# Performance work log

Hardware: AMD Instinct MI355X
Metric: run time of the kernel (lower is better)

Reference implementation:

```python
import jax, jax.numpy as jnp
import numpy as np

B = 16384
H = 1024

def setup_inputs() -> dict:
    key = jax.random.key(0)
    k1, k2, k3, k4, k5 = jax.random.split(key, 5)
    inp = jax.random.normal(k1, (B, 3 * H), dtype=jnp.float32)
    previous_state = jax.random.normal(k2, (B, H), dtype=jnp.float32)
    mask = jax.random.uniform(k3, (B,), dtype=jnp.float32)
    # params: th_normal scale 0.08
    Wur = 0.08 * jax.random.normal(k4, (H, 2 * H), dtype=jnp.float32)
    U = 0.08 * jax.random.normal(k5, (H, H), dtype=jnp.float32)
    return {"inp": inp, "previous_state": previous_state, "mask": mask, "Wur": Wur, "U": U}

def reference(inp, previous_state, mask, Wur, U):
    h = U.shape[0]
    state_inp = inp[:, :h]            # [B, H]
    gate_inp = inp[:, h:]             # [B, 2H]
    gates = jax.nn.sigmoid(previous_state @ Wur + gate_inp)  # [B, 2H]
    update = gates[:, :h]
    reset = gates[:, h:]
    p = (state_inp * reset) @ U       # [B, H]
    next_state = jnp.tanh(p + state_inp)
    # NOTE: faithful to source (additive combine, not convex blend)
    next_state_f = next_state + update + (previous_state + (1.0 - update))
    m = mask[:, None]
    return m * next_state_f + (1.0 - m) * previous_state
```

## Files before the change

### kernel.cpp

```cpp
#include <hip/hip_runtime.h>
#include <cstdint>
#include <cstddef>

#define DI __device__ __forceinline__

typedef __attribute__((ext_vector_type(8))) short short8;
typedef __attribute__((ext_vector_type(4))) float floatx4;

static constexpr int BATCH = 16384;
static constexpr int H = 1024;

DI unsigned short f32_to_bf16_bits(float x) {
  union { float f; unsigned int u; } c; c.f = x;
  unsigned int r = c.u + 0x7fffu + ((c.u >> 16) & 1u);
  return (unsigned short)(r >> 16);
}

__global__ __launch_bounds__(256) void cast_bf16_kernel(const float* __restrict__ in,
                                                        unsigned short* __restrict__ out) {
  const int i = (blockIdx.x * 256 + threadIdx.x) * 8;
  const float4 v0 = *reinterpret_cast<const float4*>(in + i);
  const float4 v1 = *reinterpret_cast<const float4*>(in + i + 4);
  short8 o;
  o[0] = (short)f32_to_bf16_bits(v0.x);
  o[1] = (short)f32_to_bf16_bits(v0.y);
  o[2] = (short)f32_to_bf16_bits(v0.z);
  o[3] = (short)f32_to_bf16_bits(v0.w);
  o[4] = (short)f32_to_bf16_bits(v1.x);
  o[5] = (short)f32_to_bf16_bits(v1.y);
  o[6] = (short)f32_to_bf16_bits(v1.z);
  o[7] = (short)f32_to_bf16_bits(v1.w);
  *reinterpret_cast<short8*>(out + i) = o;
}

__global__ __launch_bounds__(256) void transpose_cast2_kernel(const float* __restrict__ Wur,
                                                              const float* __restrict__ U,
                                                              unsigned short* __restrict__ WrT,
                                                              unsigned short* __restrict__ UT) {
  __shared__ float tile[32][33];
  const float* in;
  unsigned short* out;
  int src_stride, src_col0;
  if (blockIdx.z == 0) {
    in = Wur; out = WrT; src_stride = 2 * H; src_col0 = H;
  } else {
    in = U; out = UT; src_stride = H; src_col0 = 0;
  }
  const int bx = blockIdx.x * 32;
  const int by = blockIdx.y * 32;
  const int tx = threadIdx.x;
  const int ty = threadIdx.y;
#pragma unroll
  for (int i = 0; i < 32; i += 8)
    tile[ty + i][tx] = in[(size_t)(bx + ty + i) * src_stride + src_col0 + by + tx];
  __syncthreads();
#pragma unroll
  for (int i = 0; i < 32; i += 8)
    out[(size_t)(by + ty + i) * H + bx + tx] = f32_to_bf16_bits(tile[tx][ty + i]);
}

template <int EPI>
__global__ __launch_bounds__(256, 3) void gemm_fused(const unsigned short* __restrict__ A,
                                                     const unsigned short* __restrict__ Bt,
                                                     const float* __restrict__ inp,
                                                     const float* __restrict__ prev,
                                                     const float* __restrict__ mask,
                                                     unsigned short* __restrict__ Xout,
                                                     float* __restrict__ Out) {
  __shared__ __align__(16) unsigned short ldsA[128 * 64];
  __shared__ __align__(16) unsigned short ldsB[128 * 64];

  const int tid = threadIdx.x;
  const int lane = tid & 63;
  const int wave = tid >> 6;
  const int wm = wave >> 1;
  const int wn = wave & 1;
  const int q = lane >> 4;
  const int l16 = lane & 15;

  const int sid = blockIdx.y * gridDim.x + blockIdx.x;
  const int nwg = gridDim.x * gridDim.y;
  const int lid = (sid & 7) * (nwg >> 3) + (sid >> 3);
  const int bx = lid & 7;
  const int by = lid >> 3;
  const int blockM = by * 128;
  const int blockN = bx * 128;

  floatx4 acc[4][4] = {};

  for (int kt = 0; kt < H; kt += 64) {
#pragma unroll
    for (int j = 0; j < 4; ++j) {
      const int c = j * 256 + tid;
      const int r = c >> 3;
      const int gc = (c & 7) ^ (r & 7);
      const int cb = j * 256 + (wave << 6);
      const unsigned short* srcA = A + (size_t)(blockM + r) * H + kt + gc * 8;
      const unsigned short* srcB = Bt + (size_t)(blockN + r) * H + kt + gc * 8;
#if __has_builtin(__builtin_amdgcn_global_load_lds)
      __builtin_amdgcn_global_load_lds(
          (const __attribute__((address_space(1))) unsigned int*)srcA,
          (__attribute__((address_space(3))) unsigned int*)(&ldsA[cb * 8]), 16, 0, 0);
      __builtin_amdgcn_global_load_lds(
          (const __attribute__((address_space(1))) unsigned int*)srcB,
          (__attribute__((address_space(3))) unsigned int*)(&ldsB[cb * 8]), 16, 0, 0);
#else
      *(short8*)&ldsA[c * 8] = *(const short8*)srcA;
      *(short8*)&ldsB[c * 8] = *(const short8*)srcB;
#endif
    }
#if __has_builtin(__builtin_amdgcn_global_load_lds)
    asm volatile("s_waitcnt vmcnt(0)" ::: "memory");
#endif
    __syncthreads();

#pragma unroll
    for (int ks = 0; ks < 2; ++ks) {
      short8 af[4], bfr[4];
#pragma unroll
      for (int i = 0; i < 4; ++i) {
        const int r = wm * 64 + i * 16 + l16;
        const int ch = ks * 4 + q;
        af[i] = *(const short8*)&ldsA[(r * 8 + (ch ^ (r & 7))) * 8];
      }
#pragma unroll
      for (int j = 0; j < 4; ++j) {
        const int r = wn * 64 + j * 16 + l16;
        const int ch = ks * 4 + q;
        bfr[j] = *(const short8*)&ldsB[(r * 8 + (ch ^ (r & 7))) * 8];
      }
#pragma unroll
      for (int i = 0; i < 4; ++i)
#pragma unroll
        for (int j = 0; j < 4; ++j)
          acc[i][j] = __builtin_amdgcn_mfma_f32_16x16x32_bf16(af[i], bfr[j], acc[i][j], 0, 0, 0);
    }
    __syncthreads();
  }

#pragma unroll
  for (int i = 0; i < 4; ++i) {
    const int gr0 = blockM + wm * 64 + i * 16 + q * 4;
#pragma unroll
    for (int j = 0; j < 4; ++j) {
      const int gcol = blockN + wn * 64 + j * 16 + l16;
#pragma unroll
      for (int rg = 0; rg < 4; ++rg) {
        const int gr = gr0 + rg;
        const float v = acc[i][j][rg];
        if (EPI == 0) {
          const float z = v + inp[(size_t)gr * (3 * H) + 2 * H + gcol];
          const float rst = 1.0f / (1.0f + __expf(-z));
          const float x = inp[(size_t)gr * (3 * H) + gcol] * rst;
          Xout[(size_t)gr * H + gcol] = f32_to_bf16_bits(x);
        } else {
          const float s = inp[(size_t)gr * (3 * H) + gcol];
          const float a = v + s;
          const float ns = 1.0f - 2.0f / (__expf(2.0f * a) + 1.0f);
          const float m = mask[gr];
          Out[(size_t)gr * H + gcol] = m * (ns + 1.0f) + prev[(size_t)gr * H + gcol];
        }
      }
    }
  }
}

extern "C" void kernel_launch(void* const* d_in, const int* in_sizes, int n_in,
                              void* d_out, int out_size, void* d_ws, size_t ws_size,
                              hipStream_t stream) {
  const float* inp = (const float*)d_in[0];
  const float* prev = (const float*)d_in[1];
  const float* mask = (const float*)d_in[2];
  const float* Wur = (const float*)d_in[3];
  const float* U = (const float*)d_in[4];
  float* out = (float*)d_out;

  char* ws = (char*)d_ws;
  unsigned short* prevb = (unsigned short*)ws;
  unsigned short* Xb = (unsigned short*)(ws + (size_t)BATCH * H * 2);
  unsigned short* WrT = (unsigned short*)(ws + (size_t)BATCH * H * 4);
  unsigned short* UT = WrT + (size_t)H * H;

  cast_bf16_kernel<<<(BATCH * H) / (256 * 8), 256, 0, stream>>>(prev, prevb);
  transpose_cast2_kernel<<<dim3(H / 32, H / 32, 2), dim3(32, 8), 0, stream>>>(Wur, U, WrT, UT);

  gemm_fused<0><<<dim3(H / 128, BATCH / 128), 256, 0, stream>>>(prevb, WrT, inp, nullptr,
                                                                nullptr, Xb, nullptr);
  gemm_fused<1><<<dim3(H / 128, BATCH / 128), 256, 0, stream>>>(Xb, UT, inp, prev, mask,
                                                                nullptr, out);
}
```

Before: 427.2 us.

## Use 256x256 tiles with double-buffered LDS and interleaved load/MFMA phases

The GEMM kernels move from 128x128 tiles with 4 waves to 256x256 tiles with 8 waves. The LDS is now double-buffered and filled by direct global-to-LDS loads, so each K step overlaps the prefetch of the next tile with four MFMA quadrant phases. Those phases are separated by barriers and raised wave priority (setprio). The aim is more data reuse per tile and hidden load latency, at the cost of more registers (32 accumulators), 128KB of LDS, fewer workgroups and more barriers. Occupancy and tail effects may change as a result.

```diff
diff --git a/kernel.cpp b/kernel.cpp
--- a/kernel.cpp
+++ b/kernel.cpp
@@ -9,6 +9,8 @@
 
 static constexpr int BATCH = 16384;
 static constexpr int H = 1024;
+static constexpr int NT = H / 64;
+static constexpr int HALF = 128 * 64;
 
 DI unsigned short f32_to_bf16_bits(float x) {
   union { float f; unsigned int u; } c; c.f = x;
@@ -59,91 +61,145 @@
     out[(size_t)(by + ty + i) * H + bx + tx] = f32_to_bf16_bits(tile[tx][ty + i]);
 }
 
+DI void ld8(short8* fr, const unsigned short* base, int wofs, int l16, int q) {
+  const int x7 = l16 & 7;
+#pragma unroll
+  for (int f = 0; f < 4; ++f) {
+    const int lr = 32 * f + wofs + l16;
+#pragma unroll
+    for (int ks = 0; ks < 2; ++ks)
+      fr[f * 2 + ks] = *(const short8*)&base[lr * 64 + (((ks * 4 + q) ^ x7) * 8)];
+  }
+}
+DI void ld4(short8* fr, const unsigned short* base, int wofs, int l16, int q) {
+  const int x7 = l16 & 7;
+#pragma unroll
+  for (int jj = 0; jj < 2; ++jj) {
+    const int lc = 64 * jj + wofs + l16;
+#pragma unroll
+    for (int ks = 0; ks < 2; ++ks)
+      fr[jj * 2 + ks] = *(const short8*)&base[lc * 64 + (((ks * 4 + q) ^ x7) * 8)];
+  }
+}
+
+template <int IO, int JO>
+DI void mma16(floatx4 (&acc)[8][4], const short8* af, const short8* bf) {
+#pragma unroll
+  for (int ks = 0; ks < 2; ++ks)
+#pragma unroll
+    for (int f = 0; f < 4; ++f)
+#pragma unroll
+      for (int jj = 0; jj < 2; ++jj)
+        acc[IO + f][JO + jj] = __builtin_amdgcn_mfma_f32_16x16x32_bf16(
+            af[f * 2 + ks], bf[jj * 2 + ks], acc[IO + f][JO + jj], 0, 0, 0);
+}
+
 template <int EPI>
-__global__ __launch_bounds__(256, 3) void gemm_fused(const unsigned short* __restrict__ A,
+__global__ __launch_bounds__(512, 2) void gemm_fused(const unsigned short* __restrict__ A,
                                                      const unsigned short* __restrict__ Bt,
                                                      const float* __restrict__ inp,
                                                      const float* __restrict__ prev,
                                                      const float* __restrict__ mask,
                                                      unsigned short* __restrict__ Xout,
                                                      float* __restrict__ Out) {
-  __shared__ __align__(16) unsigned short ldsA[128 * 64];
-  __shared__ __align__(16) unsigned short ldsB[128 * 64];
+  __shared__ __align__(16) unsigned short ldsA[2 * 2 * HALF];
+  __shared__ __align__(16) unsigned short ldsB[2 * 2 * HALF];
 
   const int tid = threadIdx.x;
   const int lane = tid & 63;
-  const int wave = tid >> 6;
-  const int wm = wave >> 1;
-  const int wn = wave & 1;
+  const int w = tid >> 6;
+  const int wm16 = (w >> 2) * 16;
+  const int wn16 = (w & 3) * 16;
   const int q = lane >> 4;
   const int l16 = lane & 15;
 
   const int sid = blockIdx.y * gridDim.x + blockIdx.x;
-  const int nwg = gridDim.x * gridDim.y;
-  const int lid = (sid & 7) * (nwg >> 3) + (sid >> 3);
-  const int bx = lid & 7;
-  const int by = lid >> 3;
-  const int blockM = by * 128;
-  const int blockN = bx * 128;
-
-  floatx4 acc[4][4] = {};
-
-  for (int kt = 0; kt < H; kt += 64) {
+  const int lid = (sid & 7) * 32 + (sid >> 3);
+  const int blockN = (lid & 3) * 256;
+  const int blockM = (lid >> 2) * 256;
+
+  int srcoff[2], dstch[2];
+#pragma unroll
+  for (int n = 0; n < 2; ++n) {
+    const int c = n * 512 + tid;
+    const int r = c >> 3;
+    const int gc = (c & 7) ^ (r & 7);
+    srcoff[n] = r * H + gc * 8;
+    dstch[n] = n * 512 + w * 64;
+  }
+
+  const unsigned short* Ab = A + (size_t)blockM * H;
+  const unsigned short* Bb = Bt + (size_t)blockN * H;
+
+  auto stage = [&](const unsigned short* gsrc, unsigned short* ldst) {
+#pragma unroll
+    for (int n = 0; n < 2; ++n) {
+      __builtin_amdgcn_global_load_lds(
+          (const __attribute__((address_space(1))) unsigned int*)(gsrc + srcoff[n]),
+          (__attribute__((address_space(3))) unsigned int*)(ldst + dstch[n] * 8), 16, 0, 0);
+    }
+  };
+
+  floatx4 acc[8][4] = {};
+  short8 af[8], bf0[4], bf1[4];
+
+  stage(Ab, ldsA);
+  stage(Bb, ldsB);
+  stage(Bb + 128 * H, ldsB + HALF);
+  stage(Ab + 128 * H, ldsA + HALF);
+  asm volatile("s_waitcnt vmcnt(4)" ::: "memory");
+  __builtin_amdgcn_s_barrier();
+
+  for (int t = 0; t < NT; ++t) {
+    const int cur = t & 1;
+    const int kn = ((t + 1) & (NT - 1)) * 64;
+    const unsigned short* lAc = ldsA + cur * 2 * HALF;
+    const unsigned short* lBc = ldsB + cur * 2 * HALF;
+    unsigned short* lAn = ldsA + (cur ^ 1) * 2 * HALF;
+    unsigned short* lBn = ldsB + (cur ^ 1) * 2 * HALF;
+
+    ld8(af, lAc, wm16, l16, q);
+    ld4(bf0, lBc, wn16, l16, q);
+    stage(Ab + kn, lAn);
+    __builtin_amdgcn_s_barrier();
+    __builtin_amdgcn_s_setprio(1);
+    mma16<0, 0>(acc, af, bf0);
+    __builtin_amdgcn_s_setprio(0);
+    asm volatile("s_waitcnt vmcnt(4)" ::: "memory");
+    __builtin_amdgcn_s_barrier();
+
+    ld4(bf1, lBc + HALF, wn16, l16, q);
+    stage(Bb + kn, lBn);
+    __builtin_amdgcn_s_barrier();
+    __builtin_amdgcn_s_setprio(1);
+    mma16<0, 2>(acc, af, bf1);
+    __builtin_amdgcn_s_setprio(0);
+    asm volatile("s_waitcnt vmcnt(4)" ::: "memory");
+    __builtin_amdgcn_s_barrier();
+
+    ld8(af, lAc + HALF, wm16, l16, q);
+    stage(Bb + 128 * H + kn, lBn + HALF);
+    __builtin_amdgcn_s_barrier();
+    __builtin_amdgcn_s_setprio(1);
+    mma16<4, 2>(acc, af, bf1);
+    __builtin_amdgcn_s_setprio(0);
+    __builtin_amdgcn_s_barrier();
+
+    stage(Ab + 128 * H + kn, lAn + HALF);
+    __builtin_amdgcn_s_barrier();
+    __builtin_amdgcn_s_setprio(1);
+    mma16<4, 0>(acc, af, bf0);
+    __builtin_amdgcn_s_setprio(0);
+    asm volatile("s_waitcnt vmcnt(4)" ::: "memory");
+    __builtin_amdgcn_s_barrier();
+  }
+
+#pragma unroll
+  for (int i = 0; i < 8; ++i) {
+    const int gr0 = blockM + 128 * (i >> 2) + 32 * (i & 3) + wm16 + q * 4;
 #pragma unroll
     for (int j = 0; j < 4; ++j) {
-      const int c = j * 256 + tid;
-      const int r = c >> 3;
-      const int gc = (c & 7) ^ (r & 7);
-      const int cb = j * 256 + (wave << 6);
-      const unsigned short* srcA = A + (size_t)(blockM + r) * H + kt + gc * 8;
-      const unsigned short* srcB = Bt + (size_t)(blockN + r) * H + kt + gc * 8;
-#if __has_builtin(__builtin_amdgcn_global_load_lds)
-      __builtin_amdgcn_global_load_lds(
-          (const __attribute__((address_space(1))) unsigned int*)srcA,
-          (__attribute__((address_space(3))) unsigned int*)(&ldsA[cb * 8]), 16, 0, 0);
-      __builtin_amdgcn_global_load_lds(
-          (const __attribute__((address_space(1))) unsigned int*)srcB,
-          (__attribute__((address_space(3))) unsigned int*)(&ldsB[cb * 8]), 16, 0, 0);
-#else
-      *(short8*)&ldsA[c * 8] = *(const short8*)srcA;
-      *(short8*)&ldsB[c * 8] = *(const short8*)srcB;
-#endif
-    }
-#if __has_builtin(__builtin_amdgcn_global_load_lds)
-    asm volatile("s_waitcnt vmcnt(0)" ::: "memory");
-#endif
-    __syncthreads();
-
-#pragma unroll
-    for (int ks = 0; ks < 2; ++ks) {
-      short8 af[4], bfr[4];
-#pragma unroll
-      for (int i = 0; i < 4; ++i) {
-        const int r = wm * 64 + i * 16 + l16;
-        const int ch = ks * 4 + q;
-        af[i] = *(const short8*)&ldsA[(r * 8 + (ch ^ (r & 7))) * 8];
-      }
-#pragma unroll
-      for (int j = 0; j < 4; ++j) {
-        const int r = wn * 64 + j * 16 + l16;
-        const int ch = ks * 4 + q;
-        bfr[j] = *(const short8*)&ldsB[(r * 8 + (ch ^ (r & 7))) * 8];
-      }
-#pragma unroll
-      for (int i = 0; i < 4; ++i)
-#pragma unroll
-        for (int j = 0; j < 4; ++j)
-          acc[i][j] = __builtin_amdgcn_mfma_f32_16x16x32_bf16(af[i], bfr[j], acc[i][j], 0, 0, 0);
-    }
-    __syncthreads();
-  }
-
-#pragma unroll
-  for (int i = 0; i < 4; ++i) {
-    const int gr0 = blockM + wm * 64 + i * 16 + q * 4;
-#pragma unroll
-    for (int j = 0; j < 4; ++j) {
-      const int gcol = blockN + wn * 64 + j * 16 + l16;
+      const int gcol = blockN + 128 * (j >> 1) + 64 * (j & 1) + wn16 + l16;
 #pragma unroll
       for (int rg = 0; rg < 4; ++rg) {
         const int gr = gr0 + rg;
@@ -184,8 +240,8 @@
   cast_bf16_kernel<<<(BATCH * H) / (256 * 8), 256, 0, stream>>>(prev, prevb);
   transpose_cast2_kernel<<<dim3(H / 32, H / 32, 2), dim3(32, 8), 0, stream>>>(Wur, U, WrT, UT);
 
-  gemm_fused<0><<<dim3(H / 128, BATCH / 128), 256, 0, stream>>>(prevb, WrT, inp, nullptr,
+  gemm_fused<0><<<dim3(H / 256, BATCH / 256), 512, 0, stream>>>(prevb, WrT, inp, nullptr,
                                                                 nullptr, Xb, nullptr);
-  gemm_fused<1><<<dim3(H / 128, BATCH / 128), 256, 0, stream>>>(Xb, UT, inp, prev, mask,
+  gemm_fused<1><<<dim3(H / 256, BATCH / 256), 512, 0, stream>>>(Xb, UT, inp, prev, mask,
                                                                 nullptr, out);
 }
```

Result: no change. 422.3 us (-1.2%).
